# Performance work log

Measured on AMD Instinct MI355X. Metric: run time of the kernel, lower is better.

Reference implementation:

```python
import jax, jax.numpy as jnp
import numpy as np

HID, NH, HD = 2048, 16, 128


def setup_inputs() -> dict:
    key = jax.random.key(0)
    ks = jax.random.split(key, 9)
    B, S = 2, 2048
    std = 0.02
    return {
        "hidden_states": jax.random.normal(ks[0], (B, S, HID), dtype=jnp.float32),
        "Wq": jax.random.normal(ks[1], (HID, HID), dtype=jnp.float32) * std,
        "bq": jnp.zeros((HID,), dtype=jnp.float32),
        "Wk": jax.random.normal(ks[2], (HID, HID), dtype=jnp.float32) * std,
        "bk": jnp.zeros((HID,), dtype=jnp.float32),
        "Wv": jax.random.normal(ks[3], (HID, HID), dtype=jnp.float32) * std,
        "bv": jnp.zeros((HID,), dtype=jnp.float32),
        "Wo": jax.random.normal(ks[4], (HID, HID), dtype=jnp.float32) * std,
        "bo": jnp.zeros((HID,), dtype=jnp.float32),
    }


def reference(hidden_states, Wq, bq, Wk, bk, Wv, bv, Wo, bo):
    B, S, _ = hidden_states.shape
    # torch Linear: x @ W.T + b
    def proj(W, b):
        y = hidden_states @ W.T + b
        return y.reshape(B, S, NH, HD).transpose(0, 2, 1, 3)  # (B, NH, S, HD)

    q = proj(Wq, bq)
    k = proj(Wk, bk)
    v = proj(Wv, bv)

    scale = jnp.float32(np.sqrt(HD))
    scores = jnp.einsum("bhqd,bhkd->bhqk", q, k) / scale  # (B, NH, S, S)
    causal = jnp.triu(jnp.ones((S, S), dtype=bool), k=1)
    scores = jnp.where(causal, jnp.float32(-jnp.inf), scores)
    weights = jax.nn.softmax(scores, axis=-1)
    out = jnp.einsum("bhqk,bhkd->bhqd", weights, v)  # (B, NH, S, HD)
    out = out.transpose(0, 2, 1, 3).reshape(B, S, HID)
    return out @ Wo.T + bo
```

## Files before the change

### kernel.cpp

```cpp
#include <hip/hip_runtime.h>
#include <hip/hip_bf16.h>

#define BATCH 2
#define SEQ   2048
#define HID_  2048
#define NH_   16
#define HD_   128

typedef __bf16 bf16x8 __attribute__((ext_vector_type(8)));
typedef float  f32x4  __attribute__((ext_vector_type(4)));

__device__ __forceinline__ unsigned short f32_to_bf16(float f) {
    unsigned int u = __builtin_bit_cast(unsigned int, f);
    unsigned int r = (u + 0x7fffu + ((u >> 16) & 1u)) >> 16;
    return (unsigned short)r;
}

__device__ __forceinline__ void gld_lds16(void* lds, const void* g) {
    __builtin_amdgcn_global_load_lds(
        (const __attribute__((address_space(1))) unsigned int*)g,
        (__attribute__((address_space(3))) unsigned int*)lds, 16, 0, 0);
}

__global__ void cvt_f32_bf16(const float* __restrict__ in,
                             unsigned short* __restrict__ out, int n4) {
    int i = blockIdx.x * blockDim.x + threadIdx.x;
    if (i >= n4) return;
    float4 a = reinterpret_cast<const float4*>(in)[i];
    ushort4 o;
    o.x = f32_to_bf16(a.x);
    o.y = f32_to_bf16(a.y);
    o.z = f32_to_bf16(a.z);
    o.w = f32_to_bf16(a.w);
    reinterpret_cast<ushort4*>(out)[i] = o;
}

enum { OUT_BF16 = 0, OUT_VT = 1, OUT_F32 = 2 };

template <int MODE>
__global__ __launch_bounds__(256)
void gemm_bt(const unsigned short* __restrict__ A,
             const unsigned short* __restrict__ B,
             const float* __restrict__ bias,
             void* __restrict__ Cout,
             int M, int N, int K) {
    const int tid  = threadIdx.x;
    const int lane = tid & 63;
    const int wid  = tid >> 6;
    const int wr   = wid >> 1;
    const int wc   = wid & 1;
    const int l16  = lane & 15;
    const int l4   = lane >> 4;

    const int row0 = blockIdx.y * 128;
    const int col0 = blockIdx.x * 128;

    __shared__ unsigned short As[128 * 32];
    __shared__ unsigned short Bs[128 * 32];

    f32x4 acc[4][4] = {};

    const int srow = tid >> 2;
    const int scol = (tid & 3) * 8;
    const unsigned short* Ag = A + (size_t)(row0 + srow) * K + scol;
    const unsigned short* Bg = B + (size_t)(col0 + srow) * K + scol;
    unsigned short* AsW = As + wid * 512;
    unsigned short* BsW = Bs + wid * 512;

    const unsigned short* AsR = As + (size_t)(wr * 64 + l16) * 32 + l4 * 8;
    const unsigned short* BsR = Bs + (size_t)(wc * 64 + l16) * 32 + l4 * 8;

    for (int k0 = 0; k0 < K; k0 += 32) {
        __syncthreads();
        gld_lds16(AsW,        Ag + k0);
        gld_lds16(AsW + 2048, Ag + (size_t)64 * K + k0);
        gld_lds16(BsW,        Bg + k0);
        gld_lds16(BsW + 2048, Bg + (size_t)64 * K + k0);
        __syncthreads();

        bf16x8 af[4], bfr[4];
#pragma unroll
        for (int i = 0; i < 4; ++i)
            af[i] = *reinterpret_cast<const bf16x8*>(AsR + i * 16 * 32);
#pragma unroll
        for (int j = 0; j < 4; ++j)
            bfr[j] = *reinterpret_cast<const bf16x8*>(BsR + j * 16 * 32);
#pragma unroll
        for (int i = 0; i < 4; ++i)
#pragma unroll
            for (int j = 0; j < 4; ++j)
                acc[i][j] = __builtin_amdgcn_mfma_f32_16x16x32_bf16(
                    af[i], bfr[j], acc[i][j], 0, 0, 0);
    }

    const int wrow0 = row0 + wr * 64;
    const int wcol0 = col0 + wc * 64;
#pragma unroll
    for (int j = 0; j < 4; ++j) {
        const int col = wcol0 + j * 16 + l16;
        const float bv = bias[col];
#pragma unroll
        for (int i = 0; i < 4; ++i) {
#pragma unroll
            for (int r = 0; r < 4; ++r) {
                const int row = wrow0 + i * 16 + l4 * 4 + r;
                const float v = acc[i][j][r] + bv;
                if (MODE == OUT_BF16) {
                    ((unsigned short*)Cout)[(size_t)row * N + col] = f32_to_bf16(v);
                } else if (MODE == OUT_F32) {
                    ((float*)Cout)[(size_t)row * N + col] = v;
                } else {
                    const int b = row >> 11, s = row & (SEQ - 1);
                    const int h = col >> 7,  d = col & (HD_ - 1);
                    ((unsigned short*)Cout)[((size_t)((b * NH_ + h) * HD_ + d)) * SEQ + s] =
                        f32_to_bf16(v);
                }
            }
        }
    }
}

__global__ __launch_bounds__(256, 2)
void attn_fwd(const unsigned short* __restrict__ Qm,
              const unsigned short* __restrict__ Km,
              const unsigned short* __restrict__ Vt,
              unsigned short* __restrict__ Om) {
    const int tid  = threadIdx.x;
    const int lane = tid & 63;
    const int wq   = tid >> 6;
    const int l16  = lane & 15;
    const int l4   = lane >> 4;

    const int bh = blockIdx.x;
    const int qt = (int)gridDim.y - 1 - (int)blockIdx.y;
    const int b  = bh >> 4;
    const int h  = bh & (NH_ - 1);

    const int qbase  = qt * 64 + wq * 16;
    const int ntiles = qt + 1;

    __shared__ unsigned short Ks[2][64 * 128];
    __shared__ unsigned short Vs[2][128 * 64];
    __shared__ unsigned short plds[4][16][68];

    const unsigned short* Kbh = Km + ((size_t)b * SEQ) * HID_ + h * HD_;
    const unsigned short* Vbh = Vt + (size_t)bh * HD_ * SEQ;

    auto stage = [&](int buf, int t) {
        const int kv0 = t * 64;
        {
            const int rl = lane >> 4;
            const int ck = lane & 15;
#pragma unroll
            for (int j = 0; j < 4; ++j) {
                const int r  = wq * 16 + 4 * j + rl;
                const int lc = ck ^ (r & 7);
                gld_lds16(&Ks[buf][(wq * 16 + 4 * j) * 128],
                          Kbh + (size_t)(kv0 + r) * HID_ + lc * 8);
            }
        }
        {
            const int rl = lane >> 3;
            const int ck = lane & 7;
#pragma unroll
            for (int j = 0; j < 4; ++j) {
                const int r  = wq * 32 + 8 * j + rl;
                const int lc = ck ^ (r & 7);
                gld_lds16(&Vs[buf][(wq * 32 + 8 * j) * 64],
                          Vbh + (size_t)r * SEQ + kv0 + lc * 8);
            }
        }
    };

    stage(0, 0);
    const unsigned short* Qbase =
        Qm + ((size_t)(b * SEQ + qbase + l16)) * HID_ + h * HD_ + l4 * 8;
    bf16x8 qf[4];
#pragma unroll
    for (int kb = 0; kb < 4; ++kb)
        qf[kb] = *reinterpret_cast<const bf16x8*>(Qbase + kb * 32);

    float mrow[4], lrow[4];
#pragma unroll
    for (int r = 0; r < 4; ++r) { mrow[r] = -__builtin_inff(); lrow[r] = 0.f; }
    f32x4 acc[8] = {};

    const float scale = 0.08838834764831845f;

    int buf = 0;
    for (int t = 0; t < ntiles; ++t) {
        __syncthreads();
        if (t + 1 < ntiles) stage(buf ^ 1, t + 1);

        const unsigned short* Kb0 = &Ks[buf][0];
        const unsigned short* Vb0 = &Vs[buf][0];
        const int kv0 = t * 64;
        const int sw  = l16 & 7;

        f32x4 sc[4];
#pragma unroll
        for (int ct = 0; ct < 4; ++ct) {
            f32x4 c = {};
#pragma unroll
            for (int kb = 0; kb < 4; ++kb) {
                bf16x8 kf = *reinterpret_cast<const bf16x8*>(
                    Kb0 + (ct * 16 + l16) * 128 + ((kb * 4 + l4) ^ sw) * 8);
                c = __builtin_amdgcn_mfma_f32_16x16x32_bf16(qf[kb], kf, c, 0, 0, 0);
            }
            sc[ct] = c;
        }

        if (t == ntiles - 1) {
#pragma unroll
            for (int ct = 0; ct < 4; ++ct) {
                const int col = kv0 + ct * 16 + l16;
#pragma unroll
                for (int r = 0; r < 4; ++r) {
                    float v = sc[ct][r] * scale;
                    const int qrow = qbase + l4 * 4 + r;
                    if (col > qrow) v = -__builtin_inff();
                    sc[ct][r] = v;
                }
            }
        } else {
#pragma unroll
            for (int ct = 0; ct < 4; ++ct)
#pragma unroll
                for (int r = 0; r < 4; ++r)
                    sc[ct][r] *= scale;
        }

        float tmax[4];
#pragma unroll
        for (int r = 0; r < 4; ++r) {
            float v = fmaxf(fmaxf(sc[0][r], sc[1][r]), fmaxf(sc[2][r], sc[3][r]));
#pragma unroll
            for (int off = 8; off >= 1; off >>= 1)
                v = fmaxf(v, __shfl_xor(v, off, 64));
            tmax[r] = v;
        }

        float alpha[4], rs[4];
#pragma unroll
        for (int r = 0; r < 4; ++r) {
            const float mn = fmaxf(mrow[r], tmax[r]);
            alpha[r] = __expf(mrow[r] - mn);
            mrow[r] = mn;
            rs[r] = 0.f;
        }

#pragma unroll
        for (int ct = 0; ct < 4; ++ct) {
#pragma unroll
            for (int r = 0; r < 4; ++r) {
                const float p = __expf(sc[ct][r] - mrow[r]);
                rs[r] += p;
                plds[wq][l4 * 4 + r][ct * 16 + l16] = f32_to_bf16(p);
            }
        }

#pragma unroll
        for (int r = 0; r < 4; ++r) {
#pragma unroll
            for (int off = 8; off >= 1; off >>= 1)
                rs[r] += __shfl_xor(rs[r], off, 64);
            lrow[r] = lrow[r] * alpha[r] + rs[r];
        }

#pragma unroll
        for (int dt = 0; dt < 8; ++dt)
#pragma unroll
            for (int r = 0; r < 4; ++r)
                acc[dt][r] *= alpha[r];

        asm volatile("s_waitcnt lgkmcnt(0)" ::: "memory");
        bf16x8 pf[2];
#pragma unroll
        for (int ks = 0; ks < 2; ++ks)
            pf[ks] = *reinterpret_cast<const bf16x8*>(&plds[wq][l16][ks * 32 + l4 * 8]);
#pragma unroll
        for (int dt = 0; dt < 8; ++dt) {
#pragma unroll
            for (int ks = 0; ks < 2; ++ks) {
                bf16x8 vf = *reinterpret_cast<const bf16x8*>(
                    Vb0 + (dt * 16 + l16) * 64 + ((ks * 4 + l4) ^ sw) * 8);
                acc[dt] = __builtin_amdgcn_mfma_f32_16x16x32_bf16(pf[ks], vf, acc[dt], 0, 0, 0);
            }
        }

        buf ^= 1;
    }

    unsigned short* Ob = Om + ((size_t)(b * SEQ + qbase)) * HID_ + h * HD_;
#pragma unroll
    for (int dt = 0; dt < 8; ++dt) {
#pragma unroll
        for (int r = 0; r < 4; ++r) {
            const int qrow = l4 * 4 + r;
            const float v = acc[dt][r] / lrow[r];
            Ob[(size_t)qrow * HID_ + dt * 16 + l16] = f32_to_bf16(v);
        }
    }
}

extern "C" void kernel_launch(void* const* d_in, const int* in_sizes, int n_in,
                              void* d_out, int out_size, void* d_ws, size_t ws_size,
                              hipStream_t stream) {
    const float* X  = (const float*)d_in[0];
    const float* Wq = (const float*)d_in[1];
    const float* bq = (const float*)d_in[2];
    const float* Wk = (const float*)d_in[3];
    const float* bk = (const float*)d_in[4];
    const float* Wv = (const float*)d_in[5];
    const float* bv = (const float*)d_in[6];
    const float* Wo = (const float*)d_in[7];
    const float* bo = (const float*)d_in[8];
    float* out = (float*)d_out;

    const size_t MK = (size_t)BATCH * SEQ * HID_;
    const size_t WK = (size_t)HID_ * HID_;

    unsigned short* ws  = (unsigned short*)d_ws;
    unsigned short* Xb  = ws;
    unsigned short* Wqb = Xb  + MK;
    unsigned short* Wkb = Wqb + WK;
    unsigned short* Wvb = Wkb + WK;
    unsigned short* Wob = Wvb + WK;
    unsigned short* Qb  = Wob + WK;
    unsigned short* Kb  = Qb  + MK;
    unsigned short* Vtb = Kb  + MK;
    unsigned short* AOb = Vtb + MK;

    auto cvt = [&](const float* src, unsigned short* dst, size_t n) {
        int n4 = (int)(n / 4);
        cvt_f32_bf16<<<(n4 + 255) / 256, 256, 0, stream>>>(src, dst, n4);
    };
    cvt(X,  Xb,  MK);
    cvt(Wq, Wqb, WK);
    cvt(Wk, Wkb, WK);
    cvt(Wv, Wvb, WK);
    cvt(Wo, Wob, WK);

    const int M = BATCH * SEQ;
    dim3 g(HID_ / 128, M / 128);

    gemm_bt<OUT_BF16><<<g, 256, 0, stream>>>(Xb, Wqb, bq, Qb,  M, HID_, HID_);
    gemm_bt<OUT_BF16><<<g, 256, 0, stream>>>(Xb, Wkb, bk, Kb,  M, HID_, HID_);
    gemm_bt<OUT_VT>  <<<g, 256, 0, stream>>>(Xb, Wvb, bv, Vtb, M, HID_, HID_);

    attn_fwd<<<dim3(BATCH * NH_, SEQ / 64), 256, 0, stream>>>(Qb, Kb, Vtb, AOb);

    gemm_bt<OUT_F32><<<g, 256, 0, stream>>>(AOb, Wob, bo, out, M, HID_, HID_);
}
```

Before: 455.4 us.

## Replace 128-tile GEMM with pipelined 256-tile GEMM and fuse QKV projections

Swaps the simple 128x128 single-buffered GEMM for a 256x256-tile, 512-thread kernel. It double-buffers LDS through global_load_lds, uses an XOR-swizzled layout to avoid bank conflicts, and interleaves staging with MFMA phases using explicit barriers, waitcnt and setprio. The Q, K and V projections become one launch over a 6144-wide concatenated weight, which relies on Wq, Wk and Wv being contiguous in the buffer. This cuts launch count and raises arithmetic intensity per tile. The cost is fewer blocks for the output projection (128 tiles), heavy LDS use (128KB per block), and fragile hand-tuned synchronisation.

```diff
diff --git a/kernel.cpp b/kernel.cpp
--- a/kernel.cpp
+++ b/kernel.cpp
@@ -35,89 +35,149 @@
     reinterpret_cast<ushort4*>(out)[i] = o;
 }
 
-enum { OUT_BF16 = 0, OUT_VT = 1, OUT_F32 = 2 };
-
 template <int MODE>
-__global__ __launch_bounds__(256)
-void gemm_bt(const unsigned short* __restrict__ A,
+__global__ __launch_bounds__(512, 2)
+void gemm256(const unsigned short* __restrict__ A,
              const unsigned short* __restrict__ B,
-             const float* __restrict__ bias,
-             void* __restrict__ Cout,
-             int M, int N, int K) {
+             const float* __restrict__ bq,
+             const float* __restrict__ bk,
+             const float* __restrict__ bv,
+             unsigned short* __restrict__ Qo,
+             unsigned short* __restrict__ Ko,
+             unsigned short* __restrict__ Vto,
+             float* __restrict__ Fo) {
+    const int K = 2048;
+    const int NT = 32;
+
+    __shared__ unsigned short Asm[2][256 * 64];
+    __shared__ unsigned short Bsm[2][256 * 64];
+
     const int tid  = threadIdx.x;
     const int lane = tid & 63;
-    const int wid  = tid >> 6;
-    const int wr   = wid >> 1;
-    const int wc   = wid & 1;
+    const int w    = tid >> 6;
+    const int wm   = w >> 2;
+    const int wn   = w & 3;
     const int l16  = lane & 15;
     const int l4   = lane >> 4;
-
-    const int row0 = blockIdx.y * 128;
-    const int col0 = blockIdx.x * 128;
-
-    __shared__ unsigned short As[128 * 32];
-    __shared__ unsigned short Bs[128 * 32];
-
-    f32x4 acc[4][4] = {};
-
-    const int srow = tid >> 2;
-    const int scol = (tid & 3) * 8;
-    const unsigned short* Ag = A + (size_t)(row0 + srow) * K + scol;
-    const unsigned short* Bg = B + (size_t)(col0 + srow) * K + scol;
-    unsigned short* AsW = As + wid * 512;
-    unsigned short* BsW = Bs + wid * 512;
-
-    const unsigned short* AsR = As + (size_t)(wr * 64 + l16) * 32 + l4 * 8;
-    const unsigned short* BsR = Bs + (size_t)(wc * 64 + l16) * 32 + l4 * 8;
-
-    for (int k0 = 0; k0 < K; k0 += 32) {
-        __syncthreads();
-        gld_lds16(AsW,        Ag + k0);
-        gld_lds16(AsW + 2048, Ag + (size_t)64 * K + k0);
-        gld_lds16(BsW,        Bg + k0);
-        gld_lds16(BsW + 2048, Bg + (size_t)64 * K + k0);
-        __syncthreads();
-
-        bf16x8 af[4], bfr[4];
-#pragma unroll
-        for (int i = 0; i < 4; ++i)
-            af[i] = *reinterpret_cast<const bf16x8*>(AsR + i * 16 * 32);
-#pragma unroll
-        for (int j = 0; j < 4; ++j)
-            bfr[j] = *reinterpret_cast<const bf16x8*>(BsR + j * 16 * 32);
-#pragma unroll
-        for (int i = 0; i < 4; ++i)
-#pragma unroll
-            for (int j = 0; j < 4; ++j)
-                acc[i][j] = __builtin_amdgcn_mfma_f32_16x16x32_bf16(
-                    af[i], bfr[j], acc[i][j], 0, 0, 0);
+    const int rkey = l16 & 7;
+
+    const int row0 = blockIdx.y * 256;
+    const int col0 = blockIdx.x * 256;
+
+    const int srow8 = lane >> 3;
+    const int scol  = ((lane & 7) ^ srow8) * 8;
+    const unsigned short* Agb = A + (size_t)(row0 + w * 16 + srow8) * K + scol;
+    const unsigned short* Bgb = B + (size_t)(col0 + w * 16 + srow8) * K + scol;
+
+#define STAGE_A(bb, h, kt) do { \
+    gld_lds16(&Asm[bb][((h) * 128 + w * 16 + 0) * 64], \
+              Agb + (size_t)((h) * 128 + 0) * K + (kt) * 64); \
+    gld_lds16(&Asm[bb][((h) * 128 + w * 16 + 8) * 64], \
+              Agb + (size_t)((h) * 128 + 8) * K + (kt) * 64); \
+  } while (0)
+#define STAGE_B(bb, h, kt) do { \
+    gld_lds16(&Bsm[bb][((h) * 128 + w * 16 + 0) * 64], \
+              Bgb + (size_t)((h) * 128 + 0) * K + (kt) * 64); \
+    gld_lds16(&Bsm[bb][((h) * 128 + w * 16 + 8) * 64], \
+              Bgb + (size_t)((h) * 128 + 8) * K + (kt) * 64); \
+  } while (0)
+
+#define LDA(dst, bb, j, kk) dst = *reinterpret_cast<const bf16x8*>( \
+    &Asm[bb][(wm * 16 + (j) * 32 + l16) * 64 + ((((kk) * 4 + l4) ^ rkey) * 8)])
+#define LDB(dst, bb, jn, kk) dst = *reinterpret_cast<const bf16x8*>( \
+    &Bsm[bb][(wn * 16 + (jn) * 64 + l16) * 64 + ((((kk) * 4 + l4) ^ rkey) * 8)])
+
+    f32x4 acc[8][4] = {};
+    bf16x8 a[4][2], b[2][2];
+
+#define MM(i, j, kk) acc[i][j] = __builtin_amdgcn_mfma_f32_16x16x32_bf16( \
+    a[(i) & 3][kk], b[(j) & 1][kk], acc[i][j], 0, 0, 0)
+
+#define PH(qm, qn, bb, LA, LB, STG, VM) do { \
+    if (LA) { \
+        LDA(a[0][0], bb, (qm) * 4 + 0, 0); LDA(a[0][1], bb, (qm) * 4 + 0, 1); \
+        LDA(a[1][0], bb, (qm) * 4 + 1, 0); LDA(a[1][1], bb, (qm) * 4 + 1, 1); \
+        LDA(a[2][0], bb, (qm) * 4 + 2, 0); LDA(a[2][1], bb, (qm) * 4 + 2, 1); \
+        LDA(a[3][0], bb, (qm) * 4 + 3, 0); LDA(a[3][1], bb, (qm) * 4 + 3, 1); \
+    } \
+    if (LB) { \
+        LDB(b[0][0], bb, (qn) * 2 + 0, 0); LDB(b[0][1], bb, (qn) * 2 + 0, 1); \
+        LDB(b[1][0], bb, (qn) * 2 + 1, 0); LDB(b[1][1], bb, (qn) * 2 + 1, 1); \
+    } \
+    STG; \
+    __builtin_amdgcn_s_barrier(); \
+    asm volatile("s_waitcnt lgkmcnt(0)" ::: "memory"); \
+    __builtin_amdgcn_s_setprio(1); \
+    MM((qm) * 4 + 0, (qn) * 2 + 0, 0); MM((qm) * 4 + 0, (qn) * 2 + 0, 1); \
+    MM((qm) * 4 + 0, (qn) * 2 + 1, 0); MM((qm) * 4 + 0, (qn) * 2 + 1, 1); \
+    MM((qm) * 4 + 1, (qn) * 2 + 0, 0); MM((qm) * 4 + 1, (qn) * 2 + 0, 1); \
+    MM((qm) * 4 + 1, (qn) * 2 + 1, 0); MM((qm) * 4 + 1, (qn) * 2 + 1, 1); \
+    MM((qm) * 4 + 2, (qn) * 2 + 0, 0); MM((qm) * 4 + 2, (qn) * 2 + 0, 1); \
+    MM((qm) * 4 + 2, (qn) * 2 + 1, 0); MM((qm) * 4 + 2, (qn) * 2 + 1, 1); \
+    MM((qm) * 4 + 3, (qn) * 2 + 0, 0); MM((qm) * 4 + 3, (qn) * 2 + 0, 1); \
+    MM((qm) * 4 + 3, (qn) * 2 + 1, 0); MM((qm) * 4 + 3, (qn) * 2 + 1, 1); \
+    __builtin_amdgcn_s_setprio(0); \
+    VM; \
+    __builtin_amdgcn_s_barrier(); \
+  } while (0)
+
+    STAGE_A(0, 0, 0); STAGE_B(0, 1, 0); STAGE_A(0, 1, 0); STAGE_B(0, 0, 0);
+    STAGE_A(1, 0, 1); STAGE_B(1, 1, 1);
+    asm volatile("s_waitcnt vmcnt(4)" ::: "memory");
+    __builtin_amdgcn_s_barrier();
+
+    for (int i = 0; i < 16; ++i) {
+        const int t  = 2 * i;
+        const bool s2 = (t + 2) < NT;
+        const bool s3 = (t + 3) < NT;
+        PH(0, 0, 0, 1, 1, { STAGE_A(1, 1, t + 1); }, );
+        PH(0, 1, 0, 0, 1, { STAGE_B(1, 0, t + 1); }, );
+        PH(1, 1, 0, 1, 0, { if (s2) STAGE_A(0, 0, t + 2); }, );
+        PH(1, 0, 0, 0, 1, { if (s2) STAGE_B(0, 1, t + 2); },
+           { if (i == 15) asm volatile("s_waitcnt vmcnt(0)" ::: "memory");
+             else         asm volatile("s_waitcnt vmcnt(4)" ::: "memory"); });
+        PH(0, 0, 1, 1, 1, { if (s2) STAGE_A(0, 1, t + 2); }, );
+        PH(0, 1, 1, 0, 1, { if (s2) STAGE_B(0, 0, t + 2); }, );
+        PH(1, 1, 1, 1, 0, { if (s3) STAGE_A(1, 0, t + 3); }, );
+        PH(1, 0, 1, 0, 1, { if (s3) STAGE_B(1, 1, t + 3); },
+           { if (i < 15)  asm volatile("s_waitcnt vmcnt(4)" ::: "memory"); });
     }
-
-    const int wrow0 = row0 + wr * 64;
-    const int wcol0 = col0 + wc * 64;
-#pragma unroll
-    for (int j = 0; j < 4; ++j) {
-        const int col = wcol0 + j * 16 + l16;
-        const float bv = bias[col];
-#pragma unroll
-        for (int i = 0; i < 4; ++i) {
-#pragma unroll
-            for (int r = 0; r < 4; ++r) {
-                const int row = wrow0 + i * 16 + l4 * 4 + r;
-                const float v = acc[i][j][r] + bv;
-                if (MODE == OUT_BF16) {
-                    ((unsigned short*)Cout)[(size_t)row * N + col] = f32_to_bf16(v);
-                } else if (MODE == OUT_F32) {
-                    ((float*)Cout)[(size_t)row * N + col] = v;
+    asm volatile("s_waitcnt vmcnt(0)" ::: "memory");
+
+    const int seg = col0 >> 11;
+    const float* bias = (MODE == 2) ? bq : (seg == 0 ? bq : (seg == 1 ? bk : bv));
+#pragma unroll
+    for (int jn = 0; jn < 4; ++jn) {
+        const int col  = col0 + wn * 16 + jn * 64 + l16;
+        const int lcol = col & (HID_ - 1);
+        const float bvv = bias[lcol];
+#pragma unroll
+        for (int j = 0; j < 8; ++j) {
+#pragma unroll
+            for (int rr = 0; rr < 4; ++rr) {
+                const int row = row0 + wm * 16 + j * 32 + l4 * 4 + rr;
+                const float v = acc[j][jn][rr] + bvv;
+                if (MODE == 2) {
+                    Fo[(size_t)row * HID_ + col] = v;
+                } else if (seg == 0) {
+                    Qo[(size_t)row * HID_ + lcol] = f32_to_bf16(v);
+                } else if (seg == 1) {
+                    Ko[(size_t)row * HID_ + lcol] = f32_to_bf16(v);
                 } else {
-                    const int b = row >> 11, s = row & (SEQ - 1);
-                    const int h = col >> 7,  d = col & (HD_ - 1);
-                    ((unsigned short*)Cout)[((size_t)((b * NH_ + h) * HD_ + d)) * SEQ + s] =
+                    const int b2 = row >> 11, s = row & (SEQ - 1);
+                    const int hh = lcol >> 7, d = lcol & (HD_ - 1);
+                    Vto[((size_t)((b2 * NH_ + hh) * HD_ + d)) * SEQ + s] =
                         f32_to_bf16(v);
                 }
             }
         }
     }
+#undef STAGE_A
+#undef STAGE_B
+#undef LDA
+#undef LDB
+#undef MM
+#undef PH
 }
 
 __global__ __launch_bounds__(256, 2)
@@ -341,14 +401,11 @@
     cvt(Wv, Wvb, WK);
     cvt(Wo, Wob, WK);
 
-    const int M = BATCH * SEQ;
-    dim3 g(HID_ / 128, M / 128);
-
-    gemm_bt<OUT_BF16><<<g, 256, 0, stream>>>(Xb, Wqb, bq, Qb,  M, HID_, HID_);
-    gemm_bt<OUT_BF16><<<g, 256, 0, stream>>>(Xb, Wkb, bk, Kb,  M, HID_, HID_);
-    gemm_bt<OUT_VT>  <<<g, 256, 0, stream>>>(Xb, Wvb, bv, Vtb, M, HID_, HID_);
+    gemm256<0><<<dim3(24, 16), 512, 0, stream>>>(
+        Xb, Wqb, bq, bk, bv, Qb, Kb, Vtb, nullptr);
 
     attn_fwd<<<dim3(BATCH * NH_, SEQ / 64), 256, 0, stream>>>(Qb, Kb, Vtb, AOb);
 
-    gemm_bt<OUT_F32><<<g, 256, 0, stream>>>(AOb, Wob, bo, out, M, HID_, HID_);
-}
+    gemm256<2><<<dim3(8, 16), 512, 0, stream>>>(
+        AOb, Wob, bo, nullptr, nullptr, nullptr, nullptr, nullptr, out);
+}
```

Result: slower. 485.6 us (+6.6%).
